# Kernel optimization log

Measured on AMD Instinct MI355X. Metric: run time of the kernel, lower is better.

The kernel has to match this reference:

```python
import jax, jax.numpy as jnp
import numpy as np

B = 4096
D = 256
KERNEL_MUL = 2.0
KERNEL_NUM = 5


def setup_inputs() -> dict:
    key = jax.random.key(0)
    k1, k2 = jax.random.split(key)
    source = jax.random.normal(k1, (B, D), dtype=jnp.float32)
    target = jax.random.normal(k2, (B, D), dtype=jnp.float32)
    return {"source": source, "target": target}


def reference(source, target):
    b, d = source.shape
    n = 2 * b
    X = jnp.concatenate([source, target], axis=0)  # (2B, D)
    # pairwise squared L2 distances via quadratic expansion (avoids (2B,2B,D) intermediate)
    sq = jnp.sum(X * X, axis=1)  # (2B,)
    L2 = sq[:, None] + sq[None, :] - 2.0 * (X @ X.T)  # (2B, 2B)
    # bandwidth from detached distances (torch uses .data)
    bandwidth = jax.lax.stop_gradient(jnp.sum(L2)) / (n * n - n)
    bandwidth = bandwidth / (KERNEL_MUL ** (KERNEL_NUM // 2))  # /= 2**2
    # sum of gaussian kernels; bw_i = bandwidth * 2**i, exp(-L2 / bw_i)
    kernel_val = sum(jnp.exp(-L2 / (bandwidth * KERNEL_MUL ** i)) for i in range(KERNEL_NUM))
    # 'simple' mode: shifted-diagonal gather
    i1 = jnp.arange(b)
    i2 = (i1 + 1) % b
    loss = (kernel_val[i1, i2] + kernel_val[b + i1, b + i2]
            - kernel_val[i1, b + i2] - kernel_val[i2, b + i1])
    loss = loss / b
    return loss.sum()
```

## Files before the change

### kernel.cpp

```cpp
#include <hip/hip_runtime.h>
#include <math.h>


#define B_SZ 4096
#define D_SZ 256
#define ABLK 256

#define WS_S    8
#define WS_PART 512

__device__ __forceinline__ float dot4(float4 a, float4 b) {
    return a.x * b.x + a.y * b.y + a.z * b.z + a.w * b.w;
}

__global__ __launch_bounds__(256) void reduce_kernel(const float* __restrict__ src,
                                                     const float* __restrict__ tgt,
                                                     float* __restrict__ ws) {
    const int tid = threadIdx.x;
    const int gid = blockIdx.x * 256 + tid;
    const int cg  = tid & 63;

    const float4* S4 = (const float4*)src;
    const float4* T4 = (const float4*)tgt;

    float4 cs = make_float4(0.f, 0.f, 0.f, 0.f);
    float  sq = 0.f;
#pragma unroll
    for (int it = 0; it < 8; ++it) {
        int f   = gid + it * 65536;
        int row = f >> 6;
        float4 v = (row < B_SZ) ? S4[f] : T4[f - B_SZ * 64];
        cs.x += v.x; cs.y += v.y; cs.z += v.z; cs.w += v.w;
        sq += v.x * v.x + v.y * v.y + v.z * v.z + v.w * v.w;
    }

    for (int o = 32; o; o >>= 1) sq += __shfl_xor(sq, o, 64);

    __shared__ float4 lcs[4][64];
    __shared__ float  lsq[4];
    const int sub = tid >> 6;
    lcs[sub][cg] = cs;
    if ((tid & 63) == 0) lsq[sub] = sq;
    __syncthreads();

    if (sub == 0) {
        float4 a = lcs[0][cg], b = lcs[1][cg], c = lcs[2][cg], d = lcs[3][cg];
        float4 t = make_float4(a.x + b.x + c.x + d.x, a.y + b.y + c.y + d.y,
                               a.z + b.z + c.z + d.z, a.w + b.w + c.w + d.w);
        ((float4*)(ws + WS_PART + blockIdx.x * 256))[cg] = t;
    }
    if (tid == 0) ws[WS_S + blockIdx.x] = lsq[0] + lsq[1] + lsq[2] + lsq[3];
}

__global__ __launch_bounds__(256) void bw_kernel(float* __restrict__ ws,
                                                 float* __restrict__ out) {
    const int tid = threadIdx.x;
    const float* part = ws + WS_PART;
    float s = 0.f;
#pragma unroll 8
    for (int b = 0; b < ABLK; ++b) s += part[b * 256 + tid];
    float s2 = s * s;
    float Sp = ws[WS_S + tid];

    for (int o = 32; o; o >>= 1) {
        s2 += __shfl_xor(s2, o, 64);
        Sp += __shfl_xor(Sp, o, 64);
    }
    __shared__ float l2[4], lS[4];
    if ((tid & 63) == 0) { l2[tid >> 6] = s2; lS[tid >> 6] = Sp; }
    __syncthreads();

    if (tid == 0) {
        double norm2 = (double)l2[0] + l2[1] + l2[2] + l2[3];
        double S     = (double)lS[0] + lS[1] + lS[2] + lS[3];
        double n     = 2.0 * B_SZ;
        double sumL2 = 2.0 * n * S - 2.0 * norm2;
        double bw    = sumL2 / (n * n - n);
        bw = bw / 4.0;
#pragma unroll
        for (int k = 0; k < 5; ++k) ws[k] = (float)(1.0 / (bw * (double)(1 << k)));
        out[0] = 0.f;
    }
}

__global__ __launch_bounds__(256) void loss_kernel(const float* __restrict__ src,
                                                   const float* __restrict__ tgt,
                                                   const float* __restrict__ ws,
                                                   float* __restrict__ out) {
    const int tid  = threadIdx.x;
    const int w    = tid >> 6;
    const int lane = tid & 63;

    const float ib0 = ws[0], ib1 = ws[1], ib2 = ws[2], ib3 = ws[3], ib4 = ws[4];

    const float4* S4 = (const float4*)src;
    const float4* T4 = (const float4*)tgt;

    float wacc = 0.f;
#pragma unroll
    for (int q = 0; q < 4; ++q) {
        const int p = blockIdx.x * 16 + w * 4 + q;
        const int i = p;
        const int j = (p + 1) & (B_SZ - 1);

        float4 a = S4[i * 64 + lane];
        float4 b = S4[j * 64 + lane];
        float4 c = T4[i * 64 + lane];
        float4 d = T4[j * 64 + lane];

        float sqa = dot4(a, a), sqb = dot4(b, b), sqc = dot4(c, c), sqd = dot4(d, d);
        float ss = dot4(a, b), tt = dot4(c, d), st = dot4(a, d), ts = dot4(b, c);

        for (int o = 32; o; o >>= 1) {
            sqa += __shfl_xor(sqa, o, 64);
            sqb += __shfl_xor(sqb, o, 64);
            sqc += __shfl_xor(sqc, o, 64);
            sqd += __shfl_xor(sqd, o, 64);
            ss  += __shfl_xor(ss,  o, 64);
            tt  += __shfl_xor(tt,  o, 64);
            st  += __shfl_xor(st,  o, 64);
            ts  += __shfl_xor(ts,  o, 64);
        }

        if (lane == 0) {
            float L2ss = sqa + sqb - 2.f * ss;
            float L2tt = sqc + sqd - 2.f * tt;
            float L2st = sqa + sqd - 2.f * st;
            float L2ts = sqb + sqc - 2.f * ts;
            float k = 0.f;
            k += expf(-L2ss * ib0) + expf(-L2tt * ib0) - expf(-L2st * ib0) - expf(-L2ts * ib0);
            k += expf(-L2ss * ib1) + expf(-L2tt * ib1) - expf(-L2st * ib1) - expf(-L2ts * ib1);
            k += expf(-L2ss * ib2) + expf(-L2tt * ib2) - expf(-L2st * ib2) - expf(-L2ts * ib2);
            k += expf(-L2ss * ib3) + expf(-L2tt * ib3) - expf(-L2st * ib3) - expf(-L2ts * ib3);
            k += expf(-L2ss * ib4) + expf(-L2tt * ib4) - expf(-L2st * ib4) - expf(-L2ts * ib4);
            wacc += k;
        }
    }

    __shared__ float lacc[4];
    if (lane == 0) lacc[w] = wacc;
    __syncthreads();
    if (tid == 0) {
        float t = (lacc[0] + lacc[1] + lacc[2] + lacc[3]) * (1.0f / (float)B_SZ);
        atomicAdd(out, t);
    }
}

extern "C" void kernel_launch(void* const* d_in, const int* in_sizes, int n_in,
                              void* d_out, int out_size, void* d_ws, size_t ws_size,
                              hipStream_t stream) {
    const float* src = (const float*)d_in[0];
    const float* tgt = (const float*)d_in[1];
    float* out = (float*)d_out;
    float* ws  = (float*)d_ws;

    reduce_kernel<<<ABLK, 256, 0, stream>>>(src, tgt, ws);
    bw_kernel<<<1, 256, 0, stream>>>(ws, out);
    loss_kernel<<<B_SZ / 16, 256, 0, stream>>>(src, tgt, ws, out);
}
```

Before: 83.80 us.

## Fuse column-sum reduction with pairwise distance computation into one input pass

Merges the column-sum/norm reduction and the pair-distance computation into a single kernel that reads each source and target row once, computes the four shifted-pair L2 distances, and writes them to workspace. A single-block finish kernel then derives the bandwidth, applies the exponentials over the stored distances, and writes the output directly, without an atomic. This removes the second full read of the inputs and one kernel launch. In exchange, all exponentials run in one block, the finish kernel's workspace reads are strided per thread, and each wave now does 26 shuffle reductions.

After: 80.73 us. 1.04x faster.

```diff
diff --git a/kernel.cpp b/kernel.cpp
--- a/kernel.cpp
+++ b/kernel.cpp
@@ -3,147 +3,149 @@
 
 
 #define B_SZ 4096
-#define D_SZ 256
-#define ABLK 256
+#define NBLK 256
 
-#define WS_S    8
-#define WS_PART 512
+#define WS_SP   8
+#define WS_L2   1024
+#define WS_PART 32768
 
 __device__ __forceinline__ float dot4(float4 a, float4 b) {
     return a.x * b.x + a.y * b.y + a.z * b.z + a.w * b.w;
 }
 
-__global__ __launch_bounds__(256) void reduce_kernel(const float* __restrict__ src,
-                                                     const float* __restrict__ tgt,
-                                                     float* __restrict__ ws) {
-    const int tid = threadIdx.x;
-    const int gid = blockIdx.x * 256 + tid;
-    const int cg  = tid & 63;
+__global__ __launch_bounds__(256) void pair_reduce_kernel(const float* __restrict__ src,
+                                                          const float* __restrict__ tgt,
+                                                          float* __restrict__ ws) {
+    const int tid  = threadIdx.x;
+    const int w    = tid >> 6;
+    const int lane = tid & 63;
+    const int base = blockIdx.x * 16 + w * 4;
 
     const float4* S4 = (const float4*)src;
     const float4* T4 = (const float4*)tgt;
 
-    float4 cs = make_float4(0.f, 0.f, 0.f, 0.f);
-    float  sq = 0.f;
+    float4 a[5], c[5];
 #pragma unroll
-    for (int it = 0; it < 8; ++it) {
-        int f   = gid + it * 65536;
-        int row = f >> 6;
-        float4 v = (row < B_SZ) ? S4[f] : T4[f - B_SZ * 64];
-        cs.x += v.x; cs.y += v.y; cs.z += v.z; cs.w += v.w;
-        sq += v.x * v.x + v.y * v.y + v.z * v.z + v.w * v.w;
+    for (int q = 0; q < 5; ++q) {
+        const int r = (base + q) & (B_SZ - 1);
+        a[q] = S4[r * 64 + lane];
+        c[q] = T4[r * 64 + lane];
     }
 
-    for (int o = 32; o; o >>= 1) sq += __shfl_xor(sq, o, 64);
+    float4 cs = make_float4(0.f, 0.f, 0.f, 0.f);
+#pragma unroll
+    for (int q = 0; q < 4; ++q) {
+        cs.x += a[q].x + c[q].x;
+        cs.y += a[q].y + c[q].y;
+        cs.z += a[q].z + c[q].z;
+        cs.w += a[q].w + c[q].w;
+    }
+
+    float red[26];
+#pragma unroll
+    for (int q = 0; q < 5; ++q) {
+        red[q]     = dot4(a[q], a[q]);
+        red[5 + q] = dot4(c[q], c[q]);
+    }
+#pragma unroll
+    for (int q = 0; q < 4; ++q) {
+        red[10 + q] = dot4(a[q], a[q + 1]);
+        red[14 + q] = dot4(c[q], c[q + 1]);
+        red[18 + q] = dot4(a[q], c[q + 1]);
+        red[22 + q] = dot4(a[q + 1], c[q]);
+    }
+#pragma unroll
+    for (int r = 0; r < 26; ++r) {
+#pragma unroll
+        for (int o = 32; o; o >>= 1) red[r] += __shfl_xor(red[r], o, 64);
+    }
 
     __shared__ float4 lcs[4][64];
     __shared__ float  lsq[4];
-    const int sub = tid >> 6;
-    lcs[sub][cg] = cs;
-    if ((tid & 63) == 0) lsq[sub] = sq;
+    lcs[w][lane] = cs;
+    if (lane == 0)
+        lsq[w] = red[0] + red[1] + red[2] + red[3] + red[5] + red[6] + red[7] + red[8];
     __syncthreads();
 
-    if (sub == 0) {
-        float4 a = lcs[0][cg], b = lcs[1][cg], c = lcs[2][cg], d = lcs[3][cg];
-        float4 t = make_float4(a.x + b.x + c.x + d.x, a.y + b.y + c.y + d.y,
-                               a.z + b.z + c.z + d.z, a.w + b.w + c.w + d.w);
-        ((float4*)(ws + WS_PART + blockIdx.x * 256))[cg] = t;
+    if (w == 0) {
+        float4 x = lcs[0][lane], y = lcs[1][lane], z = lcs[2][lane], u = lcs[3][lane];
+        const int b = blockIdx.x;
+        ws[WS_PART + (4 * lane + 0) * NBLK + b] = x.x + y.x + z.x + u.x;
+        ws[WS_PART + (4 * lane + 1) * NBLK + b] = x.y + y.y + z.y + u.y;
+        ws[WS_PART + (4 * lane + 2) * NBLK + b] = x.z + y.z + z.z + u.z;
+        ws[WS_PART + (4 * lane + 3) * NBLK + b] = x.w + y.w + z.w + u.w;
+        if (lane == 0) ws[WS_SP + b] = lsq[0] + lsq[1] + lsq[2] + lsq[3];
     }
-    if (tid == 0) ws[WS_S + blockIdx.x] = lsq[0] + lsq[1] + lsq[2] + lsq[3];
+
+    if (lane == 0) {
+#pragma unroll
+        for (int q = 0; q < 4; ++q) {
+            float4 o;
+            o.x = red[q]     + red[1 + q] - 2.f * red[10 + q];
+            o.y = red[5 + q] + red[6 + q] - 2.f * red[14 + q];
+            o.z = red[q]     + red[6 + q] - 2.f * red[18 + q];
+            o.w = red[1 + q] + red[5 + q] - 2.f * red[22 + q];
+            ((float4*)(ws + WS_L2))[base + q] = o;
+        }
+    }
 }
 
-__global__ __launch_bounds__(256) void bw_kernel(float* __restrict__ ws,
-                                                 float* __restrict__ out) {
+__global__ __launch_bounds__(256) void finish_kernel(float* __restrict__ ws,
+                                                     float* __restrict__ out) {
     const int tid = threadIdx.x;
-    const float* part = ws + WS_PART;
+    const int w   = tid >> 6;
+
+    const float4* p4 = (const float4*)(ws + WS_PART);
     float s = 0.f;
 #pragma unroll 8
-    for (int b = 0; b < ABLK; ++b) s += part[b * 256 + tid];
+    for (int i = 0; i < 64; ++i) {
+        float4 v = p4[tid * 64 + i];
+        s += v.x + v.y + v.z + v.w;
+    }
     float s2 = s * s;
-    float Sp = ws[WS_S + tid];
-
+    float Sp = ws[WS_SP + tid];
+#pragma unroll
     for (int o = 32; o; o >>= 1) {
         s2 += __shfl_xor(s2, o, 64);
         Sp += __shfl_xor(Sp, o, 64);
     }
+
     __shared__ float l2[4], lS[4];
-    if ((tid & 63) == 0) { l2[tid >> 6] = s2; lS[tid >> 6] = Sp; }
+    __shared__ float sh_ib[5];
+    if ((tid & 63) == 0) { l2[w] = s2; lS[w] = Sp; }
     __syncthreads();
 
     if (tid == 0) {
         double norm2 = (double)l2[0] + l2[1] + l2[2] + l2[3];
         double S     = (double)lS[0] + lS[1] + lS[2] + lS[3];
         double n     = 2.0 * B_SZ;
-        double sumL2 = 2.0 * n * S - 2.0 * norm2;
-        double bw    = sumL2 / (n * n - n);
-        bw = bw / 4.0;
+        double bw    = (2.0 * n * S - 2.0 * norm2) / (n * n - n) / 4.0;
 #pragma unroll
-        for (int k = 0; k < 5; ++k) ws[k] = (float)(1.0 / (bw * (double)(1 << k)));
-        out[0] = 0.f;
+        for (int k = 0; k < 5; ++k) sh_ib[k] = (float)(1.0 / (bw * (double)(1 << k)));
     }
-}
+    __syncthreads();
 
-__global__ __launch_bounds__(256) void loss_kernel(const float* __restrict__ src,
-                                                   const float* __restrict__ tgt,
-                                                   const float* __restrict__ ws,
-                                                   float* __restrict__ out) {
-    const int tid  = threadIdx.x;
-    const int w    = tid >> 6;
-    const int lane = tid & 63;
+    const float ib0 = sh_ib[0], ib1 = sh_ib[1], ib2 = sh_ib[2],
+                ib3 = sh_ib[3], ib4 = sh_ib[4];
 
-    const float ib0 = ws[0], ib1 = ws[1], ib2 = ws[2], ib3 = ws[3], ib4 = ws[4];
+    const float4* L4 = (const float4*)(ws + WS_L2);
+    float acc = 0.f;
+#pragma unroll
+    for (int r = 0; r < 16; ++r) {
+        float4 q = L4[tid + r * 256];
+        acc += expf(-q.x * ib0) + expf(-q.y * ib0) - expf(-q.z * ib0) - expf(-q.w * ib0);
+        acc += expf(-q.x * ib1) + expf(-q.y * ib1) - expf(-q.z * ib1) - expf(-q.w * ib1);
+        acc += expf(-q.x * ib2) + expf(-q.y * ib2) - expf(-q.z * ib2) - expf(-q.w * ib2);
+        acc += expf(-q.x * ib3) + expf(-q.y * ib3) - expf(-q.z * ib3) - expf(-q.w * ib3);
+        acc += expf(-q.x * ib4) + expf(-q.y * ib4) - expf(-q.z * ib4) - expf(-q.w * ib4);
+    }
+#pragma unroll
+    for (int o = 32; o; o >>= 1) acc += __shfl_xor(acc, o, 64);
 
-    const float4* S4 = (const float4*)src;
-    const float4* T4 = (const float4*)tgt;
-
-    float wacc = 0.f;
-#pragma unroll
-    for (int q = 0; q < 4; ++q) {
-        const int p = blockIdx.x * 16 + w * 4 + q;
-        const int i = p;
-        const int j = (p + 1) & (B_SZ - 1);
-
-        float4 a = S4[i * 64 + lane];
-        float4 b = S4[j * 64 + lane];
-        float4 c = T4[i * 64 + lane];
-        float4 d = T4[j * 64 + lane];
-
-        float sqa = dot4(a, a), sqb = dot4(b, b), sqc = dot4(c, c), sqd = dot4(d, d);
-        float ss = dot4(a, b), tt = dot4(c, d), st = dot4(a, d), ts = dot4(b, c);
-
-        for (int o = 32; o; o >>= 1) {
-            sqa += __shfl_xor(sqa, o, 64);
-            sqb += __shfl_xor(sqb, o, 64);
-            sqc += __shfl_xor(sqc, o, 64);
-            sqd += __shfl_xor(sqd, o, 64);
-            ss  += __shfl_xor(ss,  o, 64);
-            tt  += __shfl_xor(tt,  o, 64);
-            st  += __shfl_xor(st,  o, 64);
-            ts  += __shfl_xor(ts,  o, 64);
-        }
-
-        if (lane == 0) {
-            float L2ss = sqa + sqb - 2.f * ss;
-            float L2tt = sqc + sqd - 2.f * tt;
-            float L2st = sqa + sqd - 2.f * st;
-            float L2ts = sqb + sqc - 2.f * ts;
-            float k = 0.f;
-            k += expf(-L2ss * ib0) + expf(-L2tt * ib0) - expf(-L2st * ib0) - expf(-L2ts * ib0);
-            k += expf(-L2ss * ib1) + expf(-L2tt * ib1) - expf(-L2st * ib1) - expf(-L2ts * ib1);
-            k += expf(-L2ss * ib2) + expf(-L2tt * ib2) - expf(-L2st * ib2) - expf(-L2ts * ib2);
-            k += expf(-L2ss * ib3) + expf(-L2tt * ib3) - expf(-L2st * ib3) - expf(-L2ts * ib3);
-            k += expf(-L2ss * ib4) + expf(-L2tt * ib4) - expf(-L2st * ib4) - expf(-L2ts * ib4);
-            wacc += k;
-        }
-    }
-
-    __shared__ float lacc[4];
-    if (lane == 0) lacc[w] = wacc;
+    __shared__ float la[4];
+    if ((tid & 63) == 0) la[w] = acc;
     __syncthreads();
-    if (tid == 0) {
-        float t = (lacc[0] + lacc[1] + lacc[2] + lacc[3]) * (1.0f / (float)B_SZ);
-        atomicAdd(out, t);
-    }
+    if (tid == 0) out[0] = (la[0] + la[1] + la[2] + la[3]) * (1.0f / (float)B_SZ);
 }
 
 extern "C" void kernel_launch(void* const* d_in, const int* in_sizes, int n_in,
@@ -154,7 +156,6 @@
     float* out = (float*)d_out;
     float* ws  = (float*)d_ws;
 
-    reduce_kernel<<<ABLK, 256, 0, stream>>>(src, tgt, ws);
-    bw_kernel<<<1, 256, 0, stream>>>(ws, out);
-    loss_kernel<<<B_SZ / 16, 256, 0, stream>>>(src, tgt, ws, out);
+    pair_reduce_kernel<<<NBLK, 256, 0, stream>>>(src, tgt, ws);
+    finish_kernel<<<1, 256, 0, stream>>>(ws, out);
 }
```
